# Optimization experiments

Measured on AMD Instinct MI355X. Metric: run time of the kernel, lower is better.

## Reference

```python
import math
import jax, jax.numpy as jnp
import numpy as np

HEADS = 9
EMBED = 32
TEMPERATURE = 3000.0

def _conv1x1(x, W, b):
    # x: [B,C,H,W], W: [O,C], b: [O]  (1x1 conv == channel matmul)
    return jnp.einsum('bchw,oc->bohw', x, W) + b[None, :, None, None]

def setup_inputs() -> dict:
    key = jax.random.key(0)
    ks = jax.random.split(key, 14)
    B, H, W = 2, 64, 64
    h2, w2 = 32, 32
    hd = HEADS * EMBED  # 288
    s = 0.1
    return {
        'second_frame': jax.random.normal(ks[0], (B, 3, H, W), jnp.float32),
        'first_frame_aligned': jax.random.normal(ks[1], (B, 3, H, W), jnp.float32),
        'second_frame_feat': jax.random.normal(ks[2], (B, 4, h2, w2), jnp.float32),
        'first_frame_feat_aligned': jax.random.normal(ks[3], (B, 4, h2, w2), jnp.float32),
        'Wq': jax.random.normal(ks[4], (hd, 3), jnp.float32) * s,
        'bq': jax.random.normal(ks[5], (hd,), jnp.float32) * s,
        'Wk': jax.random.normal(ks[6], (hd, 3), jnp.float32) * s,
        'bk': jax.random.normal(ks[7], (hd,), jnp.float32) * s,
        'Wv': jax.random.normal(ks[8], (hd, 4), jnp.float32) * s,
        'bv': jax.random.normal(ks[9], (hd,), jnp.float32) * s,
        'Wp': jax.random.normal(ks[10], (4, hd), jnp.float32) * s,
        'bp': jax.random.normal(ks[11], (4,), jnp.float32) * s,
        'Wt': jax.random.normal(ks[12], (1, EMBED), jnp.float32) * s,
        'bt': jax.random.normal(ks[13], (1,), jnp.float32) * s,
    }

def reference(second_frame, first_frame_aligned, second_frame_feat,
              first_frame_feat_aligned, Wq, bq, Wk, bk, Wv, bv, Wp, bp, Wt, bt):
    B, _, H, W = second_frame.shape
    HW = H * W
    # bilinear upsample of aligned features to (H, W); half-pixel centers == align_corners=False
    feat_up = jax.image.resize(first_frame_feat_aligned,
                               (B, first_frame_feat_aligned.shape[1], H, W),
                               method='linear', antialias=False)
    Q = _conv1x1(second_frame, Wq, bq).reshape(B, HEADS, EMBED, HW)
    K = _conv1x1(first_frame_aligned, Wk, bk).reshape(B, HEADS, EMBED, HW)
    V = _conv1x1(feat_up, Wv, bv).reshape(B, HEADS, EMBED, HW)
    Qn = jnp.transpose(Q, (0, 1, 3, 2))                      # [B,h,HW,d]
    sim = jnp.einsum('bhnd,bhdm->bhnm', Qn, K) / math.sqrt(EMBED)  # [B,h,HW,HW]
    # learned per-query threshold from Q
    t = jnp.einsum('bhnd,od->bhno', Qn, Wt) + bt             # [B,h,HW,1]
    attn = jax.nn.relu((sim - t) / TEMPERATURE)              # no row normalization
    out = jnp.einsum('bhnm,bhdm->bhnd', attn, V)             # [B,h,HW,d]
    out = jnp.transpose(out, (0, 1, 3, 2)).reshape(B, HEADS * EMBED, H, W)
    out_feat = _conv1x1(out, Wp, bp)                         # [B,4,H,W]
    h2, w2 = second_frame_feat.shape[-2:]
    out_feat_down = jax.image.resize(out_feat, (B, out_feat.shape[1], h2, w2),
                                     method='linear', antialias=False)
    final_feat = second_frame_feat + out_feat_down
    return final_feat, out_feat_down
```

## Files before the change

### kernel.cpp

```cpp
#include <hip/hip_runtime.h>
#include <hip/hip_bf16.h>
#include <cstddef>

#define NHEADS 9
#define D 32
#define SQ 4096
#define ZSPLIT 8
#define MBLK (SQ / ZSPLIT)
#define CHUNKS (MBLK / 64)
#define KROW 40
#define VROW 72

typedef __attribute__((ext_vector_type(8))) short bf16x8;
typedef __attribute__((ext_vector_type(4))) short bf16x4;
typedef __attribute__((ext_vector_type(4))) float f32x4;

__device__ __forceinline__ unsigned int f2bf(float f) {
    unsigned int u = __float_as_uint(f);
    u += 0x7fffu + ((u >> 16) & 1u);
    return u >> 16;
}

__device__ __forceinline__ void lds_barrier() {
    asm volatile("s_waitcnt lgkmcnt(0)\n\ts_barrier" ::: "memory");
}

__device__ __forceinline__ unsigned int trunc_pk(float lo, float hi) {
    return __builtin_amdgcn_perm(__float_as_uint(hi), __float_as_uint(lo),
                                 0x07060302u);
}

__device__ __forceinline__ bf16x8 relu_pack8(f32x4 s1, f32x4 s2) {
    union { unsigned int u[4]; bf16x8 v; } P;
    P.u[0] = trunc_pk(s1[0], s1[1]);
    P.u[1] = trunc_pk(s1[2], s1[3]);
    P.u[2] = trunc_pk(s2[0], s2[1]);
    P.u[3] = trunc_pk(s2[2], s2[3]);
    const bf16x8 z = {0, 0, 0, 0, 0, 0, 0, 0};
    return __builtin_elementwise_max(P.v, z);
}

__global__ __launch_bounds__(256) void prep_kernel(
    const float* __restrict__ x2, const float* __restrict__ x1,
    const float* __restrict__ feat1,
    const float* __restrict__ Wq, const float* __restrict__ bq,
    const float* __restrict__ Wk, const float* __restrict__ bk,
    const float* __restrict__ Wv, const float* __restrict__ bv,
    const float* __restrict__ Wt, const float* __restrict__ bt,
    unsigned short* __restrict__ Qb, unsigned short* __restrict__ Kb,
    unsigned short* __restrict__ Vt, float* __restrict__ tbuf)
{
    __shared__ unsigned short Vls[32 * 66];

    const int tid = threadIdx.x;
    int idx = blockIdx.x * blockDim.x + tid;
    int g  = idx & 3;
    int nl = tid >> 2;
    int n  = (idx >> 2) & (SQ - 1);
    int bh = idx >> 14;
    int h  = bh % NHEADS;
    int b  = bh / NHEADS;

    float xs0 = x2[((size_t)b * 3 + 0) * SQ + n];
    float xs1 = x2[((size_t)b * 3 + 1) * SQ + n];
    float xs2 = x2[((size_t)b * 3 + 2) * SQ + n];
    float ys0 = x1[((size_t)b * 3 + 0) * SQ + n];
    float ys1 = x1[((size_t)b * 3 + 1) * SQ + n];
    float ys2 = x1[((size_t)b * 3 + 2) * SQ + n];

    int yy = n >> 6, xx = n & 63;
    int jy = yy >> 1, jx = xx >> 1;
    int j0, j1, i0, i1; float wy0, wy1, wx0, wx1;
    if (yy & 1) { j0 = jy; j1 = (jy < 31) ? jy + 1 : 31; wy0 = 0.75f; wy1 = 0.25f; }
    else        { j0 = (jy > 0) ? jy - 1 : 0; j1 = jy;   wy0 = 0.25f; wy1 = 0.75f; }
    if (xx & 1) { i0 = jx; i1 = (jx < 31) ? jx + 1 : 31; wx0 = 0.75f; wx1 = 0.25f; }
    else        { i0 = (jx > 0) ? jx - 1 : 0; i1 = jx;   wx0 = 0.25f; wx1 = 0.75f; }

    float fu[4];
#pragma unroll
    for (int c = 0; c < 4; ++c) {
        const float* f = feat1 + ((size_t)b * 4 + c) * 1024;
        fu[c] = wy0 * (wx0 * f[j0 * 32 + i0] + wx1 * f[j0 * 32 + i1]) +
                wy1 * (wx0 * f[j1 * 32 + i0] + wx1 * f[j1 * 32 + i1]);
    }

    const int d0 = g * 8;
    unsigned int qp[4], kp[4];
    float tpart = 0.0f;
#pragma unroll
    for (int j = 0; j < 8; ++j) {
        int d = d0 + j, hd = h * D + d;
        float q = bq[hd] + Wq[hd * 3] * xs0 + Wq[hd * 3 + 1] * xs1 + Wq[hd * 3 + 2] * xs2;
        float k = bk[hd] + Wk[hd * 3] * ys0 + Wk[hd * 3 + 1] * ys1 + Wk[hd * 3 + 2] * ys2;
        float v = bv[hd] + Wv[hd * 4] * fu[0] + Wv[hd * 4 + 1] * fu[1] +
                  Wv[hd * 4 + 2] * fu[2] + Wv[hd * 4 + 3] * fu[3];
        tpart += q * Wt[d];
        unsigned int qb_ = f2bf(q), kb_ = f2bf(k);
        if (j & 1) { qp[j >> 1] |= qb_ << 16; kp[j >> 1] |= kb_ << 16; }
        else       { qp[j >> 1]  = qb_;       kp[j >> 1]  = kb_; }
        Vls[d * 66 + nl] = (unsigned short)f2bf(v);
    }
    tpart += __shfl_xor(tpart, 1);
    tpart += __shfl_xor(tpart, 2);
    if (g == 0) tbuf[(size_t)bh * SQ + n] = tpart + bt[0];

    size_t base = ((size_t)bh * SQ + n) * D + d0;
    *(uint4*)(Qb + base) = make_uint4(qp[0], qp[1], qp[2], qp[3]);
    *(uint4*)(Kb + base) = make_uint4(kp[0], kp[1], kp[2], kp[3]);

    __syncthreads();
    {
        int r  = tid >> 3;
        int c4 = tid & 7;
        int n0 = (blockIdx.x & 63) * 64;
        unsigned int w0 = *(const unsigned int*)&Vls[r * 66 + c4 * 4];
        unsigned int w1 = *(const unsigned int*)&Vls[r * 66 + c4 * 4 + 2];
        *(uint2*)(Vt + ((size_t)bh * D + r) * SQ + n0 + c4 * 4) = make_uint2(w0, w1);
    }
}

#define COMPUTE(KS, VS)                                                          \
    {                                                                            \
        _Pragma("unroll")                                                        \
        for (int g32 = 0; g32 < 2; ++g32) {                                      \
            const unsigned short* kbase = KS + g32 * 32 * KROW;                  \
            bf16x8 kf1 = *(const bf16x8*)(kbase + l15 * KROW + quad * 8);        \
            bf16x8 kf2 = *(const bf16x8*)(kbase + (16 + l15) * KROW + quad * 8); \
            bf16x8 vlo = *(const bf16x8*)(VS + l15 * VROW + g32 * 32 + quad * 8);\
            bf16x8 vhi = *(const bf16x8*)(VS + (l15 + 16) * VROW + g32 * 32 + quad * 8);\
            f32x4 sA1 = __builtin_amdgcn_mfma_f32_16x16x32_bf16(kf1, qfA, ciA, 0, 0, 0);\
            f32x4 sA2 = __builtin_amdgcn_mfma_f32_16x16x32_bf16(kf2, qfA, ciA, 0, 0, 0);\
            f32x4 sB1 = __builtin_amdgcn_mfma_f32_16x16x32_bf16(kf1, qfB, ciB, 0, 0, 0);\
            f32x4 sB2 = __builtin_amdgcn_mfma_f32_16x16x32_bf16(kf2, qfB, ciB, 0, 0, 0);\
            f32x4 sC1 = __builtin_amdgcn_mfma_f32_16x16x32_bf16(kf1, qfC, ciC, 0, 0, 0);\
            f32x4 sC2 = __builtin_amdgcn_mfma_f32_16x16x32_bf16(kf2, qfC, ciC, 0, 0, 0);\
            f32x4 sD1 = __builtin_amdgcn_mfma_f32_16x16x32_bf16(kf1, qfD, ciD, 0, 0, 0);\
            f32x4 sD2 = __builtin_amdgcn_mfma_f32_16x16x32_bf16(kf2, qfD, ciD, 0, 0, 0);\
            bf16x8 pA = relu_pack8(sA1, sA2);                                    \
            bf16x8 pB = relu_pack8(sB1, sB2);                                    \
            bf16x8 pC = relu_pack8(sC1, sC2);                                    \
            bf16x8 pD = relu_pack8(sD1, sD2);                                    \
            accAl = __builtin_amdgcn_mfma_f32_16x16x32_bf16(vlo, pA, accAl, 0, 0, 0);\
            accAh = __builtin_amdgcn_mfma_f32_16x16x32_bf16(vhi, pA, accAh, 0, 0, 0);\
            accBl = __builtin_amdgcn_mfma_f32_16x16x32_bf16(vlo, pB, accBl, 0, 0, 0);\
            accBh = __builtin_amdgcn_mfma_f32_16x16x32_bf16(vhi, pB, accBh, 0, 0, 0);\
            accCl = __builtin_amdgcn_mfma_f32_16x16x32_bf16(vlo, pC, accCl, 0, 0, 0);\
            accCh = __builtin_amdgcn_mfma_f32_16x16x32_bf16(vhi, pC, accCh, 0, 0, 0);\
            accDl = __builtin_amdgcn_mfma_f32_16x16x32_bf16(vlo, pD, accDl, 0, 0, 0);\
            accDh = __builtin_amdgcn_mfma_f32_16x16x32_bf16(vhi, pD, accDh, 0, 0, 0);\
        }                                                                        \
    }

__global__ __launch_bounds__(256, 4) void attn_kernel(
    const unsigned short* __restrict__ Qb,
    const unsigned short* __restrict__ Kb,
    const unsigned short* __restrict__ Vt,
    const float* __restrict__ tbuf,
    const float* __restrict__ Wp,
    float* __restrict__ ofp)
{
    __shared__ __align__(16) unsigned short Ks0[64 * KROW];
    __shared__ __align__(16) unsigned short Ks1[64 * KROW];
    __shared__ __align__(16) unsigned short Vs0[32 * VROW];
    __shared__ __align__(16) unsigned short Vs1[32 * VROW];

    const int lin  = blockIdx.x;
    const int xcd  = lin & 7;
    const int q8   = lin >> 3;
    const int xblk = q8 & 15;
    const int gl   = q8 >> 4;
    const int grp  = xcd * 18 + gl;
    const int bh   = grp >> 3;
    const int zz   = grp & 7;
    const int h    = bh % NHEADS;
    const int n0   = xblk * 256;
    const int mc0  = zz * MBLK;
    const int tid  = threadIdx.x;
    const int wave = tid >> 6;
    const int lane = tid & 63;
    const int l15  = lane & 15;
    const int quad = lane >> 4;

    const int nw = n0 + wave * 64;

    const unsigned short* qbase = Qb + ((size_t)bh * SQ + nw + l15) * D + quad * 8;
    bf16x8 qfA = *(const bf16x8*)(qbase);
    bf16x8 qfB = *(const bf16x8*)(qbase + 16 * D);
    bf16x8 qfC = *(const bf16x8*)(qbase + 32 * D);
    bf16x8 qfD = *(const bf16x8*)(qbase + 48 * D);

    const float SQRT32 = 5.656854249492381f;
    const float* tb = tbuf + (size_t)bh * SQ + nw + l15;
    float TA = tb[0]  * SQRT32;
    float TB = tb[16] * SQRT32;
    float TC = tb[32] * SQRT32;
    float TD = tb[48] * SQRT32;
    const f32x4 ciA = {-TA, -TA, -TA, -TA};
    const f32x4 ciB = {-TB, -TB, -TB, -TB};
    const f32x4 ciC = {-TC, -TC, -TC, -TC};
    const f32x4 ciD = {-TD, -TD, -TD, -TD};

    const uint4* Kg4 = (const uint4*)(Kb + (size_t)bh * SQ * D);
    const uint4* Vg4 = (const uint4*)(Vt + (size_t)bh * D * SQ);

    const int krow = tid >> 2;
    const int kcol = (tid & 3) * 8;
    const int kslot = (krow & 32) + 4 * ((krow >> 3) & 3) + (krow & 3) + ((krow & 4) << 2);
    unsigned short* kdst0 = Ks0 + kslot * KROW + kcol;
    unsigned short* kdst1 = Ks1 + kslot * KROW + kcol;
    const int vd = tid >> 3;
    const int vm = (tid & 7) * 8;
    unsigned short* vdst0 = Vs0 + vd * VROW + vm;
    unsigned short* vdst1 = Vs1 + vd * VROW + vm;
    const int vgbase = vd * (SQ / 8) + (mc0 >> 3) + (tid & 7);

    f32x4 accAl = {0.f,0.f,0.f,0.f}, accAh = {0.f,0.f,0.f,0.f};
    f32x4 accBl = {0.f,0.f,0.f,0.f}, accBh = {0.f,0.f,0.f,0.f};
    f32x4 accCl = {0.f,0.f,0.f,0.f}, accCh = {0.f,0.f,0.f,0.f};
    f32x4 accDl = {0.f,0.f,0.f,0.f}, accDh = {0.f,0.f,0.f,0.f};

    uint4 kA = Kg4[(size_t)mc0 * 4 + tid];
    uint4 vA = Vg4[vgbase];
    uint4 kB = Kg4[(size_t)(mc0 + 64) * 4 + tid];
    uint4 vB = Vg4[vgbase + 8];
    *(uint4*)kdst0 = kA;
    *(uint4*)vdst0 = vA;
    kA = Kg4[(size_t)(mc0 + 128) * 4 + tid];
    vA = Vg4[vgbase + 16];
    lds_barrier();

#pragma unroll
    for (int c = 0; c < CHUNKS; c += 2) {
        COMPUTE(Ks0, Vs0);
        *(uint4*)kdst1 = kB;
        *(uint4*)vdst1 = vB;
        {
            const int nc = (c + 3 < CHUNKS) ? c + 3 : CHUNKS - 1;
            kB = Kg4[(size_t)(mc0 + nc * 64) * 4 + tid];
            vB = Vg4[vgbase + nc * 8];
        }
        lds_barrier();

        COMPUTE(Ks1, Vs1);
        if (c + 2 < CHUNKS) {
            *(uint4*)kdst0 = kA;
            *(uint4*)vdst0 = vA;
            const int nc2 = (c + 4 < CHUNKS) ? c + 4 : CHUNKS - 1;
            kA = Kg4[(size_t)(mc0 + nc2 * 64) * 4 + tid];
            vA = Vg4[vgbase + nc2 * 8];
            lds_barrier();
        }
    }

    const float s1 = 5.892556509887896e-05f;
    const float* wph = Wp + h * D + quad * 4;
    float* obase = ofp + ((size_t)(bh * 8 + zz) * 4) * SQ + nw + l15;
#pragma unroll
    for (int o = 0; o < 4; ++o) {
        float cA = 0.f, cB = 0.f, cC = 0.f, cD = 0.f;
#pragma unroll
        for (int r = 0; r < 4; ++r) {
            float wlo = wph[o * 288 + r], whi = wph[o * 288 + 16 + r];
            cA += accAl[r] * wlo + accAh[r] * whi;
            cB += accBl[r] * wlo + accBh[r] * whi;
            cC += accCl[r] * wlo + accCh[r] * whi;
            cD += accDl[r] * wlo + accDh[r] * whi;
        }
        cA += __shfl_xor(cA, 16); cA += __shfl_xor(cA, 32);
        cB += __shfl_xor(cB, 16); cB += __shfl_xor(cB, 32);
        cC += __shfl_xor(cC, 16); cC += __shfl_xor(cC, 32);
        cD += __shfl_xor(cD, 16); cD += __shfl_xor(cD, 32);
        if (quad == 0) {
            float* ob = obase + (size_t)o * SQ;
            ob[0]  = cA * s1;
            ob[16] = cB * s1;
            ob[32] = cC * s1;
            ob[48] = cD * s1;
        }
    }
}

__global__ __launch_bounds__(256) void final_kernel(
    const float* __restrict__ ofp,
    const float* __restrict__ sff,
    const float* __restrict__ bp,
    float* __restrict__ dout)
{
    int t = blockIdx.x * 256 + threadIdx.x;
    int out = t >> 3;
    int s   = t & 7;
    int i  = out & 31;
    int jj = (out >> 5) & 31;
    int bo = out >> 10;
    int o  = bo & 3;
    int b  = bo >> 2;
    int nbase = (jj * 2) * 64 + i * 2;

    float acc = 0.0f;
#pragma unroll
    for (int h = 0; h < NHEADS; ++h) {
        const float* src = ofp +
            ((size_t)(((b * NHEADS + h) * 8 + s) * 4 + o)) * SQ + nbase;
        acc += src[0] + src[1] + src[64] + src[65];
    }
    acc += __shfl_xor(acc, 1);
    acc += __shfl_xor(acc, 2);
    acc += __shfl_xor(acc, 4);
    if (s == 0) {
        float dval = 0.25f * acc + bp[o];
        dout[out]        = sff[out] + dval;
        dout[8192 + out] = dval;
    }
}

extern "C" void kernel_launch(void* const* d_in, const int* in_sizes, int n_in,
                              void* d_out, int out_size, void* d_ws, size_t ws_size,
                              hipStream_t stream)
{
    const float* second_frame = (const float*)d_in[0];
    const float* first_frame  = (const float*)d_in[1];
    const float* sff          = (const float*)d_in[2];
    const float* ffa          = (const float*)d_in[3];
    const float* Wq = (const float*)d_in[4];
    const float* bq = (const float*)d_in[5];
    const float* Wk = (const float*)d_in[6];
    const float* bk = (const float*)d_in[7];
    const float* Wv = (const float*)d_in[8];
    const float* bv = (const float*)d_in[9];
    const float* Wp = (const float*)d_in[10];
    const float* bp = (const float*)d_in[11];
    const float* Wt = (const float*)d_in[12];
    const float* bt = (const float*)d_in[13];
    float* out = (float*)d_out;

    char* ws = (char*)d_ws;
    const size_t QKV = (size_t)2 * NHEADS * SQ * D * sizeof(unsigned short);
    unsigned short* Qb = (unsigned short*)ws;
    unsigned short* Kb = (unsigned short*)(ws + QKV);
    unsigned short* Vt = (unsigned short*)(ws + 2 * QKV);
    float* tbuf = (float*)(ws + 3 * QKV);
    float* ofp  = (float*)(ws + 3 * QKV + (size_t)2 * NHEADS * SQ * sizeof(float));

    prep_kernel<<<1152, 256, 0, stream>>>(second_frame, first_frame, ffa,
                                          Wq, bq, Wk, bk, Wv, bv, Wt, bt,
                                          Qb, Kb, Vt, tbuf);
    attn_kernel<<<16 * 18 * ZSPLIT, 256, 0, stream>>>(Qb, Kb, Vt, tbuf, Wp, ofp);
    final_kernel<<<256, 256, 0, stream>>>(ofp, sff, bp, out);
}
```

Measured before the change: 135.2 us.

## Load K/V fragments directly from global memory into registers, dropping LDS staging

The attention kernel now reads MFMA operand fragments for K and V straight from global memory into registers, double-buffered across 32-key steps. The shared-memory staging buffers and the block barriers are gone. The prep kernel writes K in the slot-permuted row order the LDS path used to apply, so the direct loads keep the same operand layout. This trades LDS traffic and synchronisation for many small, less coalesced global/L2 loads that every wave repeats, with no sharing between the four waves.

```diff
diff --git a/kernel.cpp b/kernel.cpp
--- a/kernel.cpp
+++ b/kernel.cpp
@@ -7,22 +7,15 @@
 #define SQ 4096
 #define ZSPLIT 8
 #define MBLK (SQ / ZSPLIT)
-#define CHUNKS (MBLK / 64)
-#define KROW 40
-#define VROW 72
+#define NSTEPS (MBLK / 32)
 
 typedef __attribute__((ext_vector_type(8))) short bf16x8;
-typedef __attribute__((ext_vector_type(4))) short bf16x4;
 typedef __attribute__((ext_vector_type(4))) float f32x4;
 
 __device__ __forceinline__ unsigned int f2bf(float f) {
     unsigned int u = __float_as_uint(f);
     u += 0x7fffu + ((u >> 16) & 1u);
     return u >> 16;
-}
-
-__device__ __forceinline__ void lds_barrier() {
-    asm volatile("s_waitcnt lgkmcnt(0)\n\ts_barrier" ::: "memory");
 }
 
 __device__ __forceinline__ unsigned int trunc_pk(float lo, float hi) {
@@ -104,9 +97,15 @@
     tpart += __shfl_xor(tpart, 2);
     if (g == 0) tbuf[(size_t)bh * SQ + n] = tpart + bt[0];
 
-    size_t base = ((size_t)bh * SQ + n) * D + d0;
-    *(uint4*)(Qb + base) = make_uint4(qp[0], qp[1], qp[2], qp[3]);
-    *(uint4*)(Kb + base) = make_uint4(kp[0], kp[1], kp[2], kp[3]);
+    *(uint4*)(Qb + ((size_t)bh * SQ + n) * D + d0) =
+        make_uint4(qp[0], qp[1], qp[2], qp[3]);
+
+    {
+        int nl_  = n & 63;
+        int slot = (nl_ & 32) + 4 * ((nl_ >> 3) & 3) + (nl_ & 3) + ((nl_ & 4) << 2);
+        size_t kaddr = ((size_t)bh * SQ + (n & ~63) + slot) * D + d0;
+        *(uint4*)(Kb + kaddr) = make_uint4(kp[0], kp[1], kp[2], kp[3]);
+    }
 
     __syncthreads();
     {
@@ -119,36 +118,34 @@
     }
 }
 
-#define COMPUTE(KS, VS)                                                          \
-    {                                                                            \
-        _Pragma("unroll")                                                        \
-        for (int g32 = 0; g32 < 2; ++g32) {                                      \
-            const unsigned short* kbase = KS + g32 * 32 * KROW;                  \
-            bf16x8 kf1 = *(const bf16x8*)(kbase + l15 * KROW + quad * 8);        \
-            bf16x8 kf2 = *(const bf16x8*)(kbase + (16 + l15) * KROW + quad * 8); \
-            bf16x8 vlo = *(const bf16x8*)(VS + l15 * VROW + g32 * 32 + quad * 8);\
-            bf16x8 vhi = *(const bf16x8*)(VS + (l15 + 16) * VROW + g32 * 32 + quad * 8);\
-            f32x4 sA1 = __builtin_amdgcn_mfma_f32_16x16x32_bf16(kf1, qfA, ciA, 0, 0, 0);\
-            f32x4 sA2 = __builtin_amdgcn_mfma_f32_16x16x32_bf16(kf2, qfA, ciA, 0, 0, 0);\
-            f32x4 sB1 = __builtin_amdgcn_mfma_f32_16x16x32_bf16(kf1, qfB, ciB, 0, 0, 0);\
-            f32x4 sB2 = __builtin_amdgcn_mfma_f32_16x16x32_bf16(kf2, qfB, ciB, 0, 0, 0);\
-            f32x4 sC1 = __builtin_amdgcn_mfma_f32_16x16x32_bf16(kf1, qfC, ciC, 0, 0, 0);\
-            f32x4 sC2 = __builtin_amdgcn_mfma_f32_16x16x32_bf16(kf2, qfC, ciC, 0, 0, 0);\
-            f32x4 sD1 = __builtin_amdgcn_mfma_f32_16x16x32_bf16(kf1, qfD, ciD, 0, 0, 0);\
-            f32x4 sD2 = __builtin_amdgcn_mfma_f32_16x16x32_bf16(kf2, qfD, ciD, 0, 0, 0);\
-            bf16x8 pA = relu_pack8(sA1, sA2);                                    \
-            bf16x8 pB = relu_pack8(sB1, sB2);                                    \
-            bf16x8 pC = relu_pack8(sC1, sC2);                                    \
-            bf16x8 pD = relu_pack8(sD1, sD2);                                    \
-            accAl = __builtin_amdgcn_mfma_f32_16x16x32_bf16(vlo, pA, accAl, 0, 0, 0);\
-            accAh = __builtin_amdgcn_mfma_f32_16x16x32_bf16(vhi, pA, accAh, 0, 0, 0);\
-            accBl = __builtin_amdgcn_mfma_f32_16x16x32_bf16(vlo, pB, accBl, 0, 0, 0);\
-            accBh = __builtin_amdgcn_mfma_f32_16x16x32_bf16(vhi, pB, accBh, 0, 0, 0);\
-            accCl = __builtin_amdgcn_mfma_f32_16x16x32_bf16(vlo, pC, accCl, 0, 0, 0);\
-            accCh = __builtin_amdgcn_mfma_f32_16x16x32_bf16(vhi, pC, accCh, 0, 0, 0);\
-            accDl = __builtin_amdgcn_mfma_f32_16x16x32_bf16(vlo, pD, accDl, 0, 0, 0);\
-            accDh = __builtin_amdgcn_mfma_f32_16x16x32_bf16(vhi, pD, accDh, 0, 0, 0);\
-        }                                                                        \
+#define STEP_LOAD(S, K1, K2, VL, VH)                                           \
+    K1 = *(const bf16x8*)(kbase + (size_t)(S) * (32 * D));                     \
+    K2 = *(const bf16x8*)(kbase + (size_t)(S) * (32 * D) + 16 * D);            \
+    VL = *(const bf16x8*)(vbase + (S) * 32);                                   \
+    VH = *(const bf16x8*)(vbase + (S) * 32 + 16 * SQ);
+
+#define STEP_COMPUTE(K1, K2, VL, VH)                                           \
+    {                                                                          \
+        f32x4 sA1 = __builtin_amdgcn_mfma_f32_16x16x32_bf16(K1, qfA, ciA, 0, 0, 0);\
+        f32x4 sA2 = __builtin_amdgcn_mfma_f32_16x16x32_bf16(K2, qfA, ciA, 0, 0, 0);\
+        f32x4 sB1 = __builtin_amdgcn_mfma_f32_16x16x32_bf16(K1, qfB, ciB, 0, 0, 0);\
+        f32x4 sB2 = __builtin_amdgcn_mfma_f32_16x16x32_bf16(K2, qfB, ciB, 0, 0, 0);\
+        f32x4 sC1 = __builtin_amdgcn_mfma_f32_16x16x32_bf16(K1, qfC, ciC, 0, 0, 0);\
+        f32x4 sC2 = __builtin_amdgcn_mfma_f32_16x16x32_bf16(K2, qfC, ciC, 0, 0, 0);\
+        f32x4 sD1 = __builtin_amdgcn_mfma_f32_16x16x32_bf16(K1, qfD, ciD, 0, 0, 0);\
+        f32x4 sD2 = __builtin_amdgcn_mfma_f32_16x16x32_bf16(K2, qfD, ciD, 0, 0, 0);\
+        bf16x8 pA = relu_pack8(sA1, sA2);                                      \
+        bf16x8 pB = relu_pack8(sB1, sB2);                                      \
+        bf16x8 pC = relu_pack8(sC1, sC2);                                      \
+        bf16x8 pD = relu_pack8(sD1, sD2);                                      \
+        accAl = __builtin_amdgcn_mfma_f32_16x16x32_bf16(VL, pA, accAl, 0, 0, 0);\
+        accAh = __builtin_amdgcn_mfma_f32_16x16x32_bf16(VH, pA, accAh, 0, 0, 0);\
+        accBl = __builtin_amdgcn_mfma_f32_16x16x32_bf16(VL, pB, accBl, 0, 0, 0);\
+        accBh = __builtin_amdgcn_mfma_f32_16x16x32_bf16(VH, pB, accBh, 0, 0, 0);\
+        accCl = __builtin_amdgcn_mfma_f32_16x16x32_bf16(VL, pC, accCl, 0, 0, 0);\
+        accCh = __builtin_amdgcn_mfma_f32_16x16x32_bf16(VH, pC, accCh, 0, 0, 0);\
+        accDl = __builtin_amdgcn_mfma_f32_16x16x32_bf16(VL, pD, accDl, 0, 0, 0);\
+        accDh = __builtin_amdgcn_mfma_f32_16x16x32_bf16(VH, pD, accDh, 0, 0, 0);\
     }
 
 __global__ __launch_bounds__(256, 4) void attn_kernel(
@@ -159,11 +156,6 @@
     const float* __restrict__ Wp,
     float* __restrict__ ofp)
 {
-    __shared__ __align__(16) unsigned short Ks0[64 * KROW];
-    __shared__ __align__(16) unsigned short Ks1[64 * KROW];
-    __shared__ __align__(16) unsigned short Vs0[32 * VROW];
-    __shared__ __align__(16) unsigned short Vs1[32 * VROW];
-
     const int lin  = blockIdx.x;
     const int xcd  = lin & 7;
     const int q8   = lin >> 3;
@@ -200,56 +192,25 @@
     const f32x4 ciC = {-TC, -TC, -TC, -TC};
     const f32x4 ciD = {-TD, -TD, -TD, -TD};
 
-    const uint4* Kg4 = (const uint4*)(Kb + (size_t)bh * SQ * D);
-    const uint4* Vg4 = (const uint4*)(Vt + (size_t)bh * D * SQ);
-
-    const int krow = tid >> 2;
-    const int kcol = (tid & 3) * 8;
-    const int kslot = (krow & 32) + 4 * ((krow >> 3) & 3) + (krow & 3) + ((krow & 4) << 2);
-    unsigned short* kdst0 = Ks0 + kslot * KROW + kcol;
-    unsigned short* kdst1 = Ks1 + kslot * KROW + kcol;
-    const int vd = tid >> 3;
-    const int vm = (tid & 7) * 8;
-    unsigned short* vdst0 = Vs0 + vd * VROW + vm;
-    unsigned short* vdst1 = Vs1 + vd * VROW + vm;
-    const int vgbase = vd * (SQ / 8) + (mc0 >> 3) + (tid & 7);
+    const unsigned short* kbase = Kb + ((size_t)bh * SQ + mc0 + l15) * D + quad * 8;
+    const unsigned short* vbase = Vt + ((size_t)bh * D + l15) * SQ + mc0 + quad * 8;
 
     f32x4 accAl = {0.f,0.f,0.f,0.f}, accAh = {0.f,0.f,0.f,0.f};
     f32x4 accBl = {0.f,0.f,0.f,0.f}, accBh = {0.f,0.f,0.f,0.f};
     f32x4 accCl = {0.f,0.f,0.f,0.f}, accCh = {0.f,0.f,0.f,0.f};
     f32x4 accDl = {0.f,0.f,0.f,0.f}, accDh = {0.f,0.f,0.f,0.f};
 
-    uint4 kA = Kg4[(size_t)mc0 * 4 + tid];
-    uint4 vA = Vg4[vgbase];
-    uint4 kB = Kg4[(size_t)(mc0 + 64) * 4 + tid];
-    uint4 vB = Vg4[vgbase + 8];
-    *(uint4*)kdst0 = kA;
-    *(uint4*)vdst0 = vA;
-    kA = Kg4[(size_t)(mc0 + 128) * 4 + tid];
-    vA = Vg4[vgbase + 16];
-    lds_barrier();
-
-#pragma unroll
-    for (int c = 0; c < CHUNKS; c += 2) {
-        COMPUTE(Ks0, Vs0);
-        *(uint4*)kdst1 = kB;
-        *(uint4*)vdst1 = vB;
+    bf16x8 k1a, k2a, vla, vha, k1b, k2b, vlb, vhb;
+    STEP_LOAD(0, k1a, k2a, vla, vha);
+#pragma unroll
+    for (int s = 0; s < NSTEPS; s += 2) {
+        STEP_LOAD(s + 1, k1b, k2b, vlb, vhb);
+        STEP_COMPUTE(k1a, k2a, vla, vha);
         {
-            const int nc = (c + 3 < CHUNKS) ? c + 3 : CHUNKS - 1;
-            kB = Kg4[(size_t)(mc0 + nc * 64) * 4 + tid];
-            vB = Vg4[vgbase + nc * 8];
+            const int na = (s + 2 < NSTEPS) ? s + 2 : NSTEPS - 1;
+            STEP_LOAD(na, k1a, k2a, vla, vha);
         }
-        lds_barrier();
-
-        COMPUTE(Ks1, Vs1);
-        if (c + 2 < CHUNKS) {
-            *(uint4*)kdst0 = kA;
-            *(uint4*)vdst0 = vA;
-            const int nc2 = (c + 4 < CHUNKS) ? c + 4 : CHUNKS - 1;
-            kA = Kg4[(size_t)(mc0 + nc2 * 64) * 4 + tid];
-            vA = Vg4[vgbase + nc2 * 8];
-            lds_barrier();
-        }
+        STEP_COMPUTE(k1b, k2b, vlb, vhb);
     }
 
     const float s1 = 5.892556509887896e-05f;
```

Result: slower. 162.9 us (+20.4%).
